# Kernel tuning notes

Measured on AMD Instinct MI355X. Metric: run time of the kernel, lower is better.

The kernel has to match this reference:

```python
import jax, jax.numpy as jnp
import numpy as np

B, L, H, DK, DV, DM = 8, 1024, 8, 80, 80, 640
LN_EPS = 1e-5


def setup_inputs() -> dict:
    key = jax.random.key(0)
    ks = jax.random.split(key, 5)
    q = jax.random.normal(ks[0], (B, L, DM), dtype=jnp.float32)
    k = jax.random.normal(ks[1], (B, L, DM), dtype=jnp.float32)
    v = jax.random.normal(ks[2], (B, L, DM), dtype=jnp.float32)
    # fc: nn.Linear(n_head*d_v, d_model), xavier-normal init
    fc_std = float(np.sqrt(2.0 / (H * DV + DM)))
    fc_w = jax.random.normal(ks[3], (DM, H * DV), dtype=jnp.float32) * fc_std
    fc_b = jnp.zeros((DM,), dtype=jnp.float32)
    gamma_1 = jnp.full((DM,), 1e-4, dtype=jnp.float32)  # init_values * ones(640)
    ln_w = jnp.ones((DM,), dtype=jnp.float32)
    ln_b = jnp.zeros((DM,), dtype=jnp.float32)
    return {"q": q, "k": k, "v": v, "fc_w": fc_w, "fc_b": fc_b,
            "gamma_1": gamma_1, "ln_w": ln_w, "ln_b": ln_b}


def reference(q, k, v, fc_w, fc_b, gamma_1, ln_w, ln_b):
    # Inputs are viewed directly into heads (projections are commented out in source).
    residual = q
    qh = q.reshape(B, L, H, DK)  # [b, q, h, d]
    kh = k.reshape(B, L, H, DK)  # [b, k, h, d]
    vh = v.reshape(B, L, H, DV)  # [b, k, h, d]

    # L2-distance attention scores: -sum((q-k)^2) = -(||q||^2 - 2 q.k + ||k||^2)
    sq = jnp.sum(qh * qh, axis=-1)                       # [b, q, h]
    sk = jnp.sum(kh * kh, axis=-1)                       # [b, k, h]
    cross = jnp.einsum('bqhd,bkhd->bhqk', qh, kh)        # [b, h, q, k]
    scores = -(sq.transpose(0, 2, 1)[:, :, :, None]
               - 2.0 * cross
               + sk.transpose(0, 2, 1)[:, :, None, :]) / 13.0

    attn = jax.nn.softmax(scores, axis=-1)               # softmax over keys (dim=2 in 3D view)
    # dropout(p=0.8) treated as identity (eval mode)

    out = jnp.einsum('bhqk,bkhd->bqhd', attn, vh)        # [b, q, h, dv]
    out = out.reshape(B, L, H * DV)
    out = out @ fc_w.T + fc_b                            # fc projection
    # dropout treated as identity (eval mode)

    x = out * gamma_1 + residual
    mu = jnp.mean(x, axis=-1, keepdims=True)
    var = jnp.mean((x - mu) ** 2, axis=-1, keepdims=True)
    y = (x - mu) * jax.lax.rsqrt(var + LN_EPS) * ln_w + ln_b
    return y
```

## Files before the change

kernel.cpp:

```cpp
#include <hip/hip_runtime.h>

#define B_ 8
#define L_ 1024
#define H_ 8
#define DM_ 640

typedef __attribute__((ext_vector_type(8))) short bf16x8;
typedef __attribute__((ext_vector_type(4))) short bf16x4;
typedef __attribute__((ext_vector_type(4))) float f32x4;
typedef __attribute__((ext_vector_type(2))) float f32x2;
typedef __attribute__((ext_vector_type(2))) int i32x2;
typedef __attribute__((ext_vector_type(4))) unsigned short us4;
typedef __attribute__((ext_vector_type(8))) unsigned short us8;

#if __has_builtin(__builtin_amdgcn_exp2f)
#define EXP2F __builtin_amdgcn_exp2f
#else
#define EXP2F exp2f
#endif

#define C1F 0.22195308f
#define C2F 0.11097654f

#define VTP_TILE_SHORTS 5184
#define ATTN8_OFF 10616832
#define KP_ROW_B 96

__device__ __forceinline__ unsigned short f2bf(float f) {
  unsigned int u = __builtin_bit_cast(unsigned int, f);
  u += 0x7fffu + ((u >> 16) & 1u);
  return (unsigned short)(u >> 16);
}
__device__ __forceinline__ float bf2f(unsigned short h) {
  unsigned int u = ((unsigned int)h) << 16;
  return __builtin_bit_cast(float, u);
}
__device__ __forceinline__ float sane(float x, float lim) {
  return fminf(fmaxf(x, -lim), lim);
}
__device__ __forceinline__ unsigned cvt_pk_bf16(float a, float b) {
  unsigned r;
  asm("v_cvt_pk_bf16_f32 %0, %1, %2" : "=v"(r) : "v"(a), "v"(b));
  return r;
}

__global__ __launch_bounds__(256) void prep_kernel(
    const float* __restrict__ kg, const float* __restrict__ vg,
    unsigned char* __restrict__ Kp8, unsigned short* __restrict__ Vtp) {
  __shared__ float V_lds[64 * 81];
  __shared__ float w_lds[64];
  const int tid = threadIdx.x;
  const int bh = blockIdx.x >> 4, kt = blockIdx.x & 15;
  const int b = bh >> 3, h = bh & 7;
  const int key = tid >> 2, part = tid & 3;
  const int keyg = kt * 64 + key;

  const float* krow = kg + (size_t)(b * L_ + keyg) * DM_ + h * 80 + part * 20;
  const float* vrow = vg + (size_t)(b * L_ + keyg) * DM_ + h * 80 + part * 20;
  unsigned char* kpr = Kp8 + ((size_t)bh * L_ + keyg) * KP_ROW_B + part * 20;

  float ssq = 0.f;
#pragma unroll
  for (int i = 0; i < 5; ++i) {
    float4 f = *(const float4*)(krow + 4 * i);
    ssq += f.x * f.x + f.y * f.y + f.z * f.z + f.w * f.w;
    int pk = __builtin_amdgcn_cvt_pk_fp8_f32(f.x * C1F, f.y * C1F, 0, false);
    pk = __builtin_amdgcn_cvt_pk_fp8_f32(f.z * C1F, f.w * C1F, pk, true);
    *(unsigned*)(kpr + 4 * i) = (unsigned)pk;
    float4 g4 = *(const float4*)(vrow + 4 * i);
    int d0 = part * 20 + 4 * i;
    V_lds[key * 81 + d0 + 0] = g4.x;
    V_lds[key * 81 + d0 + 1] = g4.y;
    V_lds[key * 81 + d0 + 2] = g4.z;
    V_lds[key * 81 + d0 + 3] = g4.w;
  }
  if (part == 0) {
    uint4 z = {0, 0, 0, 0};
    *(uint4*)(Kp8 + ((size_t)bh * L_ + keyg) * KP_ROW_B + 80) = z;
  }
  ssq += __shfl_xor(ssq, 1);
  ssq += __shfl_xor(ssq, 2);
  if (part == 0) w_lds[key] = EXP2F((80.f - ssq) * C2F);
  __syncthreads();

  unsigned short* vt = Vtp + (size_t)(bh * 16 + kt) * VTP_TILE_SHORTS;
#pragma unroll
  for (int r = 0; r < 11; ++r) {
    int p = r * 256 + tid;
    if (p < 81 * 32) {
      int dv = p >> 5, kp = (p & 31) * 2;
      float wa = w_lds[kp], wb = w_lds[kp + 1];
      float va = (dv < 80) ? V_lds[kp * 81 + dv] * wa : wa;
      float vb = (dv < 80) ? V_lds[(kp + 1) * 81 + dv] * wb : wb;
      *(unsigned*)(vt + dv * 64 + kp) =
          (unsigned)f2bf(va) | ((unsigned)f2bf(vb) << 16);
    }
  }
}

#define KSTRB 112
#define VSTR 76

__global__ __launch_bounds__(256, 4) void attn_kernel(
    const float* __restrict__ qg, const unsigned char* __restrict__ Kp8,
    const unsigned short* __restrict__ Vtp, unsigned char* __restrict__ attn8) {
  __shared__ __align__(16) unsigned char K_lds[2][64 * KSTRB];
  __shared__ __align__(16) unsigned short Vt_lds[2][80 * VSTR];
  __shared__ __align__(16) unsigned short w_sh[2][64];

  const int tid = threadIdx.x;
  const int wid = tid >> 6, lane = tid & 63;
  const int col = lane & 15, g = lane >> 4;
  const int bx = blockIdx.x;
  const int bh = bx & 63, qt = bx >> 6;
  const int b = bh >> 3, h = bh & 7;

  const int kf0 = tid, kf1 = tid + 256;
  const int kr0 = kf0 / 6, kc0 = kf0 - kr0 * 6;
  const int kr1 = kf1 / 6, kc1 = kf1 - kr1 * 6;
  const int va0 = tid, va1 = tid + 256, va2 = tid + 512;
  const int vr0 = va0 >> 3, vc0 = va0 & 7;
  const int vr1 = va1 >> 3, vc1 = va1 & 7;
  const int vr2 = va2 >> 3, vc2 = va2 & 7;

  const unsigned char* kslice = Kp8 + (size_t)bh * L_ * KP_ROW_B;
  const unsigned short* vslice = Vtp + (size_t)(bh * 16) * VTP_TILE_SHORTS;

  uint4 sk0, sk1;
  us8 sv0, sv1, sv2, sw;
  auto load_tile = [&](int kt) {
    const unsigned char* kb = kslice + (size_t)kt * 64 * KP_ROW_B;
    const unsigned short* vb = vslice + (size_t)kt * VTP_TILE_SHORTS;
    sk0 = *(const uint4*)(kb + kr0 * KP_ROW_B + kc0 * 16);
    if (tid < 128) sk1 = *(const uint4*)(kb + kr1 * KP_ROW_B + kc1 * 16);
    sv0 = *(const us8*)(vb + vr0 * 64 + vc0 * 8);
    sv1 = *(const us8*)(vb + vr1 * 64 + vc1 * 8);
    if (tid < 128) sv2 = *(const us8*)(vb + vr2 * 64 + vc2 * 8);
    if (tid < 8) sw = *(const us8*)(vb + 5120 + tid * 8);
  };
  auto write_tile = [&](int bf) {
    *(uint4*)&K_lds[bf][kr0 * KSTRB + kc0 * 16] = sk0;
    if (tid < 128) *(uint4*)&K_lds[bf][kr1 * KSTRB + kc1 * 16] = sk1;
    *(us8*)&Vt_lds[bf][vr0 * VSTR + vc0 * 8] = sv0;
    *(us8*)&Vt_lds[bf][vr1 * VSTR + vc1 * 8] = sv1;
    if (tid < 128) *(us8*)&Vt_lds[bf][vr2 * VSTR + vc2 * 8] = sv2;
    if (tid < 8) *(us8*)&w_sh[bf][tid * 8] = sw;
  };

  long qa[3];
  {
    const int qrow = qt * 64 + wid * 16 + col;
    const float* qr = qg + (size_t)(b * L_ + qrow) * DM_ + h * 80;
#pragma unroll
    for (int c = 0; c < 3; ++c) {
      int d0 = c * 32 + g * 8;
      if (d0 < 80) {
        float4 f0 = *(const float4*)(qr + d0);
        float4 f1 = *(const float4*)(qr + d0 + 4);
        int lo = __builtin_amdgcn_cvt_pk_fp8_f32(f0.x, f0.y, 0, false);
        lo = __builtin_amdgcn_cvt_pk_fp8_f32(f0.z, f0.w, lo, true);
        int hi = __builtin_amdgcn_cvt_pk_fp8_f32(f1.x, f1.y, 0, false);
        hi = __builtin_amdgcn_cvt_pk_fp8_f32(f1.z, f1.w, hi, true);
        i32x2 q2 = {lo, hi};
        qa[c] = __builtin_bit_cast(long, q2);
      } else {
        qa[c] = 0;
      }
    }
  }

  f32x4 acc_o[5];
#pragma unroll
  for (int u = 0; u < 5; ++u) {
    f32x4 z = {0.f, 0.f, 0.f, 0.f};
    acc_o[u] = z;
  }
  float lp = 0.f;

  load_tile(0);
  write_tile(0);
  __syncthreads();

  for (int kt = 0; kt < 16; ++kt) {
    const int cur = kt & 1;
    if (kt < 15) load_tile(kt + 1);

    f32x4 accS[4];
#pragma unroll
    for (int t = 0; t < 4; ++t) {
      f32x4 z = {0.f, 0.f, 0.f, 0.f};
      accS[t] = z;
    }
#pragma unroll
    for (int t = 0; t < 4; ++t) {
      const unsigned char* tb = &K_lds[cur][(t * 16 + col) * KSTRB];
      long k0 = *(const long*)(tb + g * 8);
      long k1 = *(const long*)(tb + 32 + g * 8);
      long k2 = *(const long*)(tb + 64 + g * 8);
      accS[t] = __builtin_amdgcn_mfma_f32_16x16x32_fp8_fp8(k0, qa[0], accS[t], 0, 0, 0);
      accS[t] = __builtin_amdgcn_mfma_f32_16x16x32_fp8_fp8(k1, qa[1], accS[t], 0, 0, 0);
      accS[t] = __builtin_amdgcn_mfma_f32_16x16x32_fp8_fp8(k2, qa[2], accS[t], 0, 0, 0);
    }

#pragma unroll
    for (int t = 0; t < 4; ++t) {
      us4 w4 = *(const us4*)&w_sh[cur][t * 16 + g * 4];
      float w0 = bf2f(w4[0]), w1 = bf2f(w4[1]), w2 = bf2f(w4[2]), w3 = bf2f(w4[3]);
      float p0 = EXP2F(accS[t][0]), p1 = EXP2F(accS[t][1]);
      float p2 = EXP2F(accS[t][2]), p3 = EXP2F(accS[t][3]);
      lp += p0 * w0 + p1 * w1 + p2 * w2 + p3 * w3;
      i32x2 pw = {(int)cvt_pk_bf16(p0, p1), (int)cvt_pk_bf16(p2, p3)};
      bf16x4 pf = __builtin_bit_cast(bf16x4, pw);
#pragma unroll
      for (int u = 0; u < 5; ++u) {
        bf16x4 vf = *(const bf16x4*)&Vt_lds[cur][(u * 16 + col) * VSTR + t * 16 + g * 4];
        acc_o[u] = __builtin_amdgcn_mfma_f32_16x16x16bf16_1k(vf, pf, acc_o[u], 0, 0, 0);
      }
    }

    if (kt < 15) {
      write_tile(cur ^ 1);
      __syncthreads();
    }
  }

  float l = lp + __shfl_xor(lp, 16);
  l += __shfl_xor(l, 32);
  float invl = 1.0f / fmaxf(l, 1e-30f);
  const int qrow = qt * 64 + wid * 16 + col;
  unsigned char* ob = attn8 + (size_t)(b * L_ + qrow) * DM_ + h * 80;
#pragma unroll
  for (int u = 0; u < 5; ++u) {
    float o0 = sane(acc_o[u][0] * invl, 240.f);
    float o1 = sane(acc_o[u][1] * invl, 240.f);
    float o2 = sane(acc_o[u][2] * invl, 240.f);
    float o3 = sane(acc_o[u][3] * invl, 240.f);
    int pk = __builtin_amdgcn_cvt_pk_fp8_f32(o0, o1, 0, false);
    pk = __builtin_amdgcn_cvt_pk_fp8_f32(o2, o3, pk, true);
    *(int*)(ob + u * 16 + g * 4) = pk;
  }
}

#define BSTR 40
__global__ __launch_bounds__(256) void fc_kernel(
    const unsigned char* __restrict__ attn8, const float* __restrict__ w,
    const float* __restrict__ fcb, const float* __restrict__ gamma,
    const float* __restrict__ qres, unsigned short* __restrict__ xout) {
  __shared__ __align__(16) unsigned short A_lds[2][64 * BSTR];
  __shared__ __align__(16) unsigned short B_lds[2][64 * BSTR];

  const int tid = threadIdx.x;
  const int wid = tid >> 6, lane = tid & 63;
  const int col = lane & 15, g = lane >> 4;
  const int rt = blockIdx.x / 10, cn = blockIdx.x % 10;
  const int wm = wid >> 1, wn = wid & 1;
  const int r = tid >> 2, sg = tid & 3;

  f32x4 acc[2][2];
#pragma unroll
  for (int m = 0; m < 2; ++m)
#pragma unroll
    for (int n = 0; n < 2; ++n) {
      f32x4 z = {0.f, 0.f, 0.f, 0.f};
      acc[m][n] = z;
    }

  uint2 sa;
  float4 sb0, sb1;
  auto load_k = [&](int kc) {
    sa = *(const uint2*)(attn8 + (size_t)(rt * 64 + r) * DM_ + kc * 32 + sg * 8);
    const float* wsrc = w + (size_t)(cn * 64 + r) * DM_ + kc * 32 + sg * 8;
    sb0 = *(const float4*)wsrc;
    sb1 = *(const float4*)(wsrc + 4);
  };
  auto write_k = [&](int bf) {
    const unsigned* adw = (const unsigned*)&sa;
    unsigned ow[4];
#pragma unroll
    for (int d = 0; d < 2; ++d) {
      f32x2 lo = __builtin_amdgcn_cvt_pk_f32_fp8(adw[d], false);
      f32x2 hi = __builtin_amdgcn_cvt_pk_f32_fp8(adw[d], true);
      ow[2 * d] = cvt_pk_bf16(lo[0], lo[1]);
      ow[2 * d + 1] = cvt_pk_bf16(hi[0], hi[1]);
    }
    *(uint4*)&A_lds[bf][r * BSTR + sg * 8] = *(const uint4*)ow;
    unsigned bw[4] = {cvt_pk_bf16(sb0.x, sb0.y), cvt_pk_bf16(sb0.z, sb0.w),
                      cvt_pk_bf16(sb1.x, sb1.y), cvt_pk_bf16(sb1.z, sb1.w)};
    *(uint4*)&B_lds[bf][r * BSTR + sg * 8] = *(const uint4*)bw;
  };

  load_k(0);
  write_k(0);
  __syncthreads();

  for (int kc = 0; kc < 20; ++kc) {
    const int cur = kc & 1;
    if (kc < 19) load_k(kc + 1);

    bf16x8 af[2], bfr[2];
#pragma unroll
    for (int m = 0; m < 2; ++m)
      af[m] = *(const bf16x8*)&A_lds[cur][(wm * 32 + m * 16 + col) * BSTR + g * 8];
#pragma unroll
    for (int n = 0; n < 2; ++n)
      bfr[n] = *(const bf16x8*)&B_lds[cur][(wn * 32 + n * 16 + col) * BSTR + g * 8];
#pragma unroll
    for (int m = 0; m < 2; ++m)
#pragma unroll
      for (int n = 0; n < 2; ++n)
        acc[m][n] = __builtin_amdgcn_mfma_f32_16x16x32_bf16(af[m], bfr[n], acc[m][n], 0, 0, 0);

    if (kc < 19) {
      write_k(cur ^ 1);
      __syncthreads();
    }
  }

  int jcol[2];
  float fb2[2], gm[2];
#pragma unroll
  for (int n = 0; n < 2; ++n) {
    jcol[n] = cn * 64 + wn * 32 + n * 16 + col;
    fb2[n] = fcb[jcol[n]];
    gm[n] = gamma[jcol[n]];
  }
#pragma unroll
  for (int m = 0; m < 2; ++m) {
    int rowg = rt * 64 + wm * 32 + m * 16 + g * 4;
#pragma unroll
    for (int j = 0; j < 4; ++j) {
      int row = rowg + j;
#pragma unroll
      for (int n = 0; n < 2; ++n) {
        float xv = (acc[m][n][j] + fb2[n]) * gm[n] + qres[(size_t)row * DM_ + jcol[n]];
        xout[(size_t)row * DM_ + jcol[n]] = f2bf(sane(xv, 1e5f));
      }
    }
  }
}

__global__ __launch_bounds__(256) void ln_kernel(
    const unsigned short* __restrict__ x, const float* __restrict__ lw,
    const float* __restrict__ lb, float* __restrict__ y) {
  const int wid = threadIdx.x >> 6, lane = threadIdx.x & 63;
  const int row = blockIdx.x * 4 + wid;
  const unsigned short* xr = x + (size_t)row * DM_;

  unsigned int u[5];
  float s = 0.f, ss = 0.f;
#pragma unroll
  for (int i = 0; i < 5; ++i) {
    u[i] = *(const unsigned int*)(xr + 2 * (lane + 64 * i));
    float a0 = bf2f((unsigned short)(u[i] & 0xffff));
    float a1 = bf2f((unsigned short)(u[i] >> 16));
    s += a0 + a1;
    ss += a0 * a0 + a1 * a1;
  }
#pragma unroll
  for (int d = 1; d < 64; d <<= 1) {
    s += __shfl_xor(s, d);
    ss += __shfl_xor(ss, d);
  }
  const float mu = s * (1.f / 640.f);
  const float var = ss * (1.f / 640.f) - mu * mu;
  const float rstd = rsqrtf(var + 1e-5f);

  float* yr = y + (size_t)row * DM_;
#pragma unroll
  for (int i = 0; i < 5; ++i) {
    int c0 = 2 * (lane + 64 * i);
    float a0 = bf2f((unsigned short)(u[i] & 0xffff));
    float a1 = bf2f((unsigned short)(u[i] >> 16));
    float2 wv = *(const float2*)(lw + c0);
    float2 bv = *(const float2*)(lb + c0);
    float2 out;
    out.x = (a0 - mu) * rstd * wv.x + bv.x;
    out.y = (a1 - mu) * rstd * wv.y + bv.y;
    *(float2*)(yr + c0) = out;
  }
}

extern "C" void kernel_launch(void* const* d_in, const int* in_sizes, int n_in,
                              void* d_out, int out_size, void* d_ws, size_t ws_size,
                              hipStream_t stream) {
  const float* q = (const float*)d_in[0];
  const float* k = (const float*)d_in[1];
  const float* v = (const float*)d_in[2];
  const float* fw = (const float*)d_in[3];
  const float* fb = (const float*)d_in[4];
  const float* g1 = (const float*)d_in[5];
  const float* lw = (const float*)d_in[6];
  const float* lb = (const float*)d_in[7];

  unsigned short* vtp = (unsigned short*)d_out;
  unsigned char* attn8 = (unsigned char*)d_out + ATTN8_OFF;
  unsigned char* kp8 = (unsigned char*)d_ws;
  unsigned short* xws = (unsigned short*)d_ws;
  float* y = (float*)d_out;

  prep_kernel<<<dim3(64 * 16), dim3(256), 0, stream>>>(k, v, kp8, vtp);
  attn_kernel<<<dim3(64 * 16), dim3(256), 0, stream>>>(q, kp8, vtp, attn8);
  fc_kernel<<<dim3(128 * 10), dim3(256), 0, stream>>>(attn8, fw, fb, g1, q, xws);
  ln_kernel<<<dim3(8192 / 4), dim3(256), 0, stream>>>(xws, lw, lb, y);
}
```

Baseline: 84.75 us.

## Split attention warps across query and key subtiles with LDS partial-sum reduction

```diff
diff --git a/kernel.cpp b/kernel.cpp
--- a/kernel.cpp
+++ b/kernel.cpp
@@ -101,7 +101,7 @@
 #define KSTRB 112
 #define VSTR 76
 
-__global__ __launch_bounds__(256, 4) void attn_kernel(
+__global__ __launch_bounds__(256, 3) void attn_kernel(
     const float* __restrict__ qg, const unsigned char* __restrict__ Kp8,
     const unsigned short* __restrict__ Vtp, unsigned char* __restrict__ attn8) {
   __shared__ __align__(16) unsigned char K_lds[2][64 * KSTRB];
@@ -111,6 +111,7 @@
   const int tid = threadIdx.x;
   const int wid = tid >> 6, lane = tid & 63;
   const int col = lane & 15, g = lane >> 4;
+  const int kw = wid >> 1, qw = wid & 1;
   const int bx = blockIdx.x;
   const int bh = bx & 63, qt = bx >> 6;
   const int b = bh >> 3, h = bh & 7;
@@ -147,35 +148,40 @@
     if (tid < 8) *(us8*)&w_sh[bf][tid * 8] = sw;
   };
 
-  long qa[3];
+  long qa[2][3];
   {
-    const int qrow = qt * 64 + wid * 16 + col;
-    const float* qr = qg + (size_t)(b * L_ + qrow) * DM_ + h * 80;
-#pragma unroll
-    for (int c = 0; c < 3; ++c) {
-      int d0 = c * 32 + g * 8;
-      if (d0 < 80) {
-        float4 f0 = *(const float4*)(qr + d0);
-        float4 f1 = *(const float4*)(qr + d0 + 4);
-        int lo = __builtin_amdgcn_cvt_pk_fp8_f32(f0.x, f0.y, 0, false);
-        lo = __builtin_amdgcn_cvt_pk_fp8_f32(f0.z, f0.w, lo, true);
-        int hi = __builtin_amdgcn_cvt_pk_fp8_f32(f1.x, f1.y, 0, false);
-        hi = __builtin_amdgcn_cvt_pk_fp8_f32(f1.z, f1.w, hi, true);
-        i32x2 q2 = {lo, hi};
-        qa[c] = __builtin_bit_cast(long, q2);
-      } else {
-        qa[c] = 0;
-      }
-    }
-  }
-
-  f32x4 acc_o[5];
-#pragma unroll
-  for (int u = 0; u < 5; ++u) {
-    f32x4 z = {0.f, 0.f, 0.f, 0.f};
-    acc_o[u] = z;
-  }
-  float lp = 0.f;
+#pragma unroll
+    for (int j = 0; j < 2; ++j) {
+      const int qrow = qt * 64 + (qw * 2 + j) * 16 + col;
+      const float* qr = qg + (size_t)(b * L_ + qrow) * DM_ + h * 80;
+#pragma unroll
+      for (int c = 0; c < 3; ++c) {
+        int d0 = c * 32 + g * 8;
+        if (d0 < 80) {
+          float4 f0 = *(const float4*)(qr + d0);
+          float4 f1 = *(const float4*)(qr + d0 + 4);
+          int lo = __builtin_amdgcn_cvt_pk_fp8_f32(f0.x, f0.y, 0, false);
+          lo = __builtin_amdgcn_cvt_pk_fp8_f32(f0.z, f0.w, lo, true);
+          int hi = __builtin_amdgcn_cvt_pk_fp8_f32(f1.x, f1.y, 0, false);
+          hi = __builtin_amdgcn_cvt_pk_fp8_f32(f1.z, f1.w, hi, true);
+          i32x2 q2 = {lo, hi};
+          qa[j][c] = __builtin_bit_cast(long, q2);
+        } else {
+          qa[j][c] = 0;
+        }
+      }
+    }
+  }
+
+  f32x4 acc_o[2][5];
+#pragma unroll
+  for (int j = 0; j < 2; ++j)
+#pragma unroll
+    for (int u = 0; u < 5; ++u) {
+      f32x4 z = {0.f, 0.f, 0.f, 0.f};
+      acc_o[j][u] = z;
+    }
+  float lp[2] = {0.f, 0.f};
 
   load_tile(0);
   write_tile(0);
@@ -185,36 +191,48 @@
     const int cur = kt & 1;
     if (kt < 15) load_tile(kt + 1);
 
-    f32x4 accS[4];
-#pragma unroll
-    for (int t = 0; t < 4; ++t) {
-      f32x4 z = {0.f, 0.f, 0.f, 0.f};
-      accS[t] = z;
-    }
-#pragma unroll
-    for (int t = 0; t < 4; ++t) {
+    f32x4 accS[2][2];
+#pragma unroll
+    for (int j = 0; j < 2; ++j)
+#pragma unroll
+      for (int i = 0; i < 2; ++i) {
+        f32x4 z = {0.f, 0.f, 0.f, 0.f};
+        accS[j][i] = z;
+      }
+#pragma unroll
+    for (int i = 0; i < 2; ++i) {
+      const int t = kw * 2 + i;
       const unsigned char* tb = &K_lds[cur][(t * 16 + col) * KSTRB];
       long k0 = *(const long*)(tb + g * 8);
       long k1 = *(const long*)(tb + 32 + g * 8);
       long k2 = *(const long*)(tb + 64 + g * 8);
-      accS[t] = __builtin_amdgcn_mfma_f32_16x16x32_fp8_fp8(k0, qa[0], accS[t], 0, 0, 0);
-      accS[t] = __builtin_amdgcn_mfma_f32_16x16x32_fp8_fp8(k1, qa[1], accS[t], 0, 0, 0);
-      accS[t] = __builtin_amdgcn_mfma_f32_16x16x32_fp8_fp8(k2, qa[2], accS[t], 0, 0, 0);
-    }
-
-#pragma unroll
-    for (int t = 0; t < 4; ++t) {
+#pragma unroll
+      for (int j = 0; j < 2; ++j) {
+        accS[j][i] = __builtin_amdgcn_mfma_f32_16x16x32_fp8_fp8(k0, qa[j][0], accS[j][i], 0, 0, 0);
+        accS[j][i] = __builtin_amdgcn_mfma_f32_16x16x32_fp8_fp8(k1, qa[j][1], accS[j][i], 0, 0, 0);
+        accS[j][i] = __builtin_amdgcn_mfma_f32_16x16x32_fp8_fp8(k2, qa[j][2], accS[j][i], 0, 0, 0);
+      }
+    }
+
+#pragma unroll
+    for (int i = 0; i < 2; ++i) {
+      const int t = kw * 2 + i;
       us4 w4 = *(const us4*)&w_sh[cur][t * 16 + g * 4];
       float w0 = bf2f(w4[0]), w1 = bf2f(w4[1]), w2 = bf2f(w4[2]), w3 = bf2f(w4[3]);
-      float p0 = EXP2F(accS[t][0]), p1 = EXP2F(accS[t][1]);
-      float p2 = EXP2F(accS[t][2]), p3 = EXP2F(accS[t][3]);
-      lp += p0 * w0 + p1 * w1 + p2 * w2 + p3 * w3;
-      i32x2 pw = {(int)cvt_pk_bf16(p0, p1), (int)cvt_pk_bf16(p2, p3)};
-      bf16x4 pf = __builtin_bit_cast(bf16x4, pw);
+      bf16x4 pf[2];
+#pragma unroll
+      for (int j = 0; j < 2; ++j) {
+        float p0 = EXP2F(accS[j][i][0]), p1 = EXP2F(accS[j][i][1]);
+        float p2 = EXP2F(accS[j][i][2]), p3 = EXP2F(accS[j][i][3]);
+        lp[j] += p0 * w0 + p1 * w1 + p2 * w2 + p3 * w3;
+        i32x2 pw = {(int)cvt_pk_bf16(p0, p1), (int)cvt_pk_bf16(p2, p3)};
+        pf[j] = __builtin_bit_cast(bf16x4, pw);
+      }
 #pragma unroll
       for (int u = 0; u < 5; ++u) {
         bf16x4 vf = *(const bf16x4*)&Vt_lds[cur][(u * 16 + col) * VSTR + t * 16 + g * 4];
-        acc_o[u] = __builtin_amdgcn_mfma_f32_16x16x16bf16_1k(vf, pf, acc_o[u], 0, 0, 0);
+        acc_o[0][u] = __builtin_amdgcn_mfma_f32_16x16x16bf16_1k(vf, pf[0], acc_o[0][u], 0, 0, 0);
+        acc_o[1][u] = __builtin_amdgcn_mfma_f32_16x16x16bf16_1k(vf, pf[1], acc_o[1][u], 0, 0, 0);
       }
     }
 
@@ -224,20 +242,49 @@
     }
   }
 
-  float l = lp + __shfl_xor(lp, 16);
-  l += __shfl_xor(l, 32);
-  float invl = 1.0f / fmaxf(l, 1e-30f);
-  const int qrow = qt * 64 + wid * 16 + col;
-  unsigned char* ob = attn8 + (size_t)(b * L_ + qrow) * DM_ + h * 80;
-#pragma unroll
-  for (int u = 0; u < 5; ++u) {
-    float o0 = sane(acc_o[u][0] * invl, 240.f);
-    float o1 = sane(acc_o[u][1] * invl, 240.f);
-    float o2 = sane(acc_o[u][2] * invl, 240.f);
-    float o3 = sane(acc_o[u][3] * invl, 240.f);
-    int pk = __builtin_amdgcn_cvt_pk_fp8_f32(o0, o1, 0, false);
-    pk = __builtin_amdgcn_cvt_pk_fp8_f32(o2, o3, pk, true);
-    *(int*)(ob + u * 16 + g * 4) = pk;
+  float* scr = (float*)&Vt_lds[0][0];
+  float* my = scr + (qw * 64 + lane) * 44;
+  __syncthreads();
+  if (kw == 1) {
+#pragma unroll
+    for (int j = 0; j < 2; ++j)
+#pragma unroll
+      for (int u = 0; u < 5; ++u)
+        *(f32x4*)(my + (j * 5 + u) * 4) = acc_o[j][u];
+    f32x4 lv = {lp[0], lp[1], 0.f, 0.f};
+    *(f32x4*)(my + 40) = lv;
+  }
+  __syncthreads();
+  if (kw == 0) {
+#pragma unroll
+    for (int j = 0; j < 2; ++j)
+#pragma unroll
+      for (int u = 0; u < 5; ++u) {
+        f32x4 pv = *(const f32x4*)(my + (j * 5 + u) * 4);
+        acc_o[j][u] += pv;
+      }
+    f32x4 lv = *(const f32x4*)(my + 40);
+    lp[0] += lv[0];
+    lp[1] += lv[1];
+
+#pragma unroll
+    for (int j = 0; j < 2; ++j) {
+      float l = lp[j] + __shfl_xor(lp[j], 16);
+      l += __shfl_xor(l, 32);
+      float invl = 1.0f / fmaxf(l, 1e-30f);
+      const int qrow = qt * 64 + (qw * 2 + j) * 16 + col;
+      unsigned char* ob = attn8 + (size_t)(b * L_ + qrow) * DM_ + h * 80;
+#pragma unroll
+      for (int u = 0; u < 5; ++u) {
+        float o0 = sane(acc_o[j][u][0] * invl, 240.f);
+        float o1 = sane(acc_o[j][u][1] * invl, 240.f);
+        float o2 = sane(acc_o[j][u][2] * invl, 240.f);
+        float o3 = sane(acc_o[j][u][3] * invl, 240.f);
+        int pk = __builtin_amdgcn_cvt_pk_fp8_f32(o0, o1, 0, false);
+        pk = __builtin_amdgcn_cvt_pk_fp8_f32(o2, o3, pk, true);
+        *(int*)(ob + u * 16 + g * 4) = pk;
+      }
+    }
   }
 }
 
```

Measured after the change: 84.15 us. About the same (-0.7%).
